# Performance work log

Measured on AMD Instinct MI355X. Metric: run time of the kernel, lower is better.

## Reference

```python
import jax, jax.numpy as jnp
import numpy as np

B, G, K = 16, 5000, 256
NUM_CELLS, HID = 100, 64
STEPS, ALPHA = 10, 0.1


def setup_inputs() -> dict:
    key = jax.random.key(0)
    ks = jax.random.split(key, 10)
    ctl = jax.random.normal(ks[0], (B, G), dtype=jnp.float32)
    drug_targets = jax.random.uniform(ks[1], (B, G), dtype=jnp.float32)
    cell_idx = jax.random.randint(ks[2], (B,), 0, NUM_CELLS)
    drug_fp = jax.random.normal(ks[3], (B, 128), dtype=jnp.float32)
    # gene->module membership matrix (constructor constant M_gk)
    M = jax.random.uniform(ks[4], (G, K), dtype=jnp.float32)
    # module-module adjacency (constructor constant A_kk), column-normalized for stability
    A = jax.random.uniform(ks[5], (K, K), dtype=jnp.float32)
    A = A / jnp.sum(A, axis=0, keepdims=True)
    # shared Dense(hidden_dim, relu): input feature dim is 3 (ctl, t, z_gene stacked)
    W1 = jax.random.normal(ks[6], (3, HID), dtype=jnp.float32) * 0.5
    b1 = jnp.zeros((HID,), dtype=jnp.float32)
    cell_emb = jax.random.normal(ks[7], (NUM_CELLS, HID), dtype=jnp.float32) * 0.05
    W2 = jax.random.normal(ks[8], (HID, 1), dtype=jnp.float32) * 0.1
    b2 = jnp.zeros((1,), dtype=jnp.float32)
    return {"ctl": ctl, "drug_targets": drug_targets, "cell_idx": cell_idx,
            "drug_fp": drug_fp, "M": M, "A": A, "W1": W1, "b1": b1,
            "cell_emb": cell_emb, "W2": W2, "b2": b2}


def reference(ctl, drug_targets, cell_idx, drug_fp, M, A, W1, b1, cell_emb, W2, b2):
    t = drug_targets                                   # [B, G]
    # max-pool gene targets into modules: max_g t[b,g] * M[g,k]
    t_mod = jnp.max(t[:, :, None] * M[None, :, :], axis=1)   # [B, K]
    # APPNP propagation: Z = (1-alpha) * Z @ A + alpha * S, fixed 10 steps
    Z = t_mod
    for _ in range(STEPS):
        Z = (1.0 - ALPHA) * (Z @ A) + ALPHA * t_mod
    z_gene = Z @ M.T                                   # [B, G]
    x = jnp.stack([ctl, t, z_gene], axis=-1)           # [B, G, 3]
    h = jax.nn.relu(x @ W1 + b1)                       # [B, G, HID]
    h = h + cell_emb[cell_idx][:, None, :]             # broadcast cell embedding
    y = jnp.squeeze(h @ W2 + b2, axis=-1)              # [B, G]
    return y
```

## Files before the change

kernel.cpp:

```cpp
#include <hip/hip_runtime.h>

#define G 5000
#define K 256
#define BATCH 16
#define HID 64
#define STEPS 10
#define NC 125
#define GPER 40

__global__ void maxpool_kernel(const float* __restrict__ t,
                               const float* __restrict__ M,
                               const float* __restrict__ A,
                               float* __restrict__ partials,
                               float* __restrict__ awarm) {
    __shared__ float tl[GPER][8];
    const int c  = blockIdx.x >> 1;
    const int bg = blockIdx.x & 1;
    const int b0 = bg * 8;
    const int k  = threadIdx.x;
    const int g0 = c * GPER;

    float4 aw = make_float4(0.f, 0.f, 0.f, 0.f);
    if (k < 64)
        aw = ((const float4*)A)[((size_t)blockIdx.x * 64 + k) & 16383];

    for (int i = k; i < GPER * 8; i += 256) {
        int gi = i >> 3, b = i & 7;
        tl[gi][b] = t[(b0 + b) * G + g0 + gi];
    }
    __syncthreads();

    float mx[8];
#pragma unroll
    for (int b = 0; b < 8; ++b) mx[b] = 0.f;

#pragma unroll 4
    for (int gi = 0; gi < GPER; ++gi) {
        float mg = M[(size_t)(g0 + gi) * K + k];
#pragma unroll
        for (int b = 0; b < 8; ++b)
            mx[b] = fmaxf(mx[b], tl[gi][b] * mg);
    }
#pragma unroll
    for (int b = 0; b < 8; ++b)
        partials[((size_t)c * BATCH + b0 + b) * K + k] = mx[b];

    if (k < 64) awarm[k] = aw.x + aw.y + aw.z + aw.w;
}

__global__ __launch_bounds__(1024, 4)
void appnp_fused(const float* __restrict__ partials,
                 const float* __restrict__ A,
                 const int* __restrict__ cell_idx,
                 const float* __restrict__ cell_emb,
                 const float* __restrict__ W2,
                 const float* __restrict__ b2,
                 float* __restrict__ Zfin,
                 float* __restrict__ ce_dot) {
    __shared__ float4 zb[2][K / 4];
    __shared__ float  Sm[K];
    __shared__ float  red[4][K];
    __shared__ float  ce_red[HID];

    const int b  = blockIdx.x;
    const int t  = threadIdx.x;
    const int k  = t & 255;
    const int jc = t >> 8;
    const int j0 = jc * 64;

    float Areg[64];
#pragma unroll
    for (int jj = 0; jj < 64; ++jj)
        Areg[jj] = A[(size_t)(j0 + jj) * K + k];

    {
        int c0 = jc * 32, c1 = min(NC, c0 + 32);
        float m = 0.f;
        for (int c = c0; c < c1; ++c)
            m = fmaxf(m, partials[((size_t)c * BATCH + b) * K + k]);
        red[jc][k] = m;
    }
    if (t < HID) {
        int ci = cell_idx[b];
        ce_red[t] = cell_emb[ci * HID + t] * W2[t];
    }
    __syncthreads();
    if (jc == 0) {
        float s = fmaxf(fmaxf(red[0][k], red[1][k]), fmaxf(red[2][k], red[3][k]));
        Sm[k] = s;
        ((float*)zb)[k] = s;
    }
    if (t == 0) {
        float s = b2[0];
        for (int h = 0; h < HID; ++h) s += ce_red[h];
        ce_dot[b] = s;
    }
    __syncthreads();

    for (int s = 0; s < STEPS; ++s) {
        const float4* cur4 = zb[s & 1] + (j0 >> 2);
        float*        nxt  = (float*)zb[(s + 1) & 1];
        float acc = 0.f;
#pragma unroll
        for (int q = 0; q < 16; ++q) {
            float4 c4 = cur4[q];
            acc = fmaf(c4.x, Areg[4 * q + 0], acc);
            acc = fmaf(c4.y, Areg[4 * q + 1], acc);
            acc = fmaf(c4.z, Areg[4 * q + 2], acc);
            acc = fmaf(c4.w, Areg[4 * q + 3], acc);
        }
        red[jc][k] = acc;
        __syncthreads();
        if (jc == 0)
            nxt[k] = 0.9f * (red[0][k] + red[1][k] + red[2][k] + red[3][k])
                   + 0.1f * Sm[k];
        __syncthreads();
    }
    if (jc == 0) Zfin[b * K + k] = ((float*)zb)[k];
}

__global__ void final_kernel(const float* __restrict__ ctl,
                             const float* __restrict__ t_in,
                             const float* __restrict__ Z,
                             const float* __restrict__ M,
                             const float* __restrict__ W1,
                             const float* __restrict__ b1,
                             const float* __restrict__ W2,
                             const float* __restrict__ ce_dot,
                             float* __restrict__ out) {
    __shared__ float4 zl[BATCH * (K / 4)];
    __shared__ float4 wpack[HID];
    __shared__ float  w2l[HID];
    __shared__ float  cel[BATCH];

    const int t = threadIdx.x;
    const float4* Z4 = (const float4*)Z;
    for (int i = t; i < BATCH * (K / 4); i += 256) zl[i] = Z4[i];
    if (t < HID) {
        wpack[t] = make_float4(W1[t], W1[HID + t], W1[2 * HID + t], b1[t]);
        w2l[t] = W2[t];
    }
    if (t < BATCH) cel[t] = ce_dot[t];
    __syncthreads();

    const int gl = t & 63;
    const int bg = t >> 6;
    const int g = blockIdx.x * 64 + gl;
    if (g >= G) return;

    float acc[4] = {0.f, 0.f, 0.f, 0.f};
    const float4* M4 = (const float4*)(M + (size_t)g * K);
#pragma unroll 4
    for (int k4 = 0; k4 < K / 4; ++k4) {
        float4 m4 = M4[k4];
#pragma unroll
        for (int i = 0; i < 4; ++i) {
            float4 z4 = zl[(bg * 4 + i) * (K / 4) + k4];
            acc[i] = fmaf(m4.x, z4.x, acc[i]);
            acc[i] = fmaf(m4.y, z4.y, acc[i]);
            acc[i] = fmaf(m4.z, z4.z, acc[i]);
            acc[i] = fmaf(m4.w, z4.w, acc[i]);
        }
    }

    float cv[4], tv[4], y[4];
#pragma unroll
    for (int i = 0; i < 4; ++i) {
        int b = bg * 4 + i;
        cv[i] = ctl[b * G + g];
        tv[i] = t_in[b * G + g];
        y[i] = cel[b];
    }
#pragma unroll 4
    for (int h = 0; h < HID; ++h) {
        float4 w = wpack[h];
        float w2h = w2l[h];
#pragma unroll
        for (int i = 0; i < 4; ++i) {
            float pre = w.w;
            pre = fmaf(cv[i], w.x, pre);
            pre = fmaf(tv[i], w.y, pre);
            pre = fmaf(acc[i], w.z, pre);
            pre = fmaxf(pre, 0.f);
            y[i] = fmaf(pre, w2h, y[i]);
        }
    }
#pragma unroll
    for (int i = 0; i < 4; ++i)
        out[(bg * 4 + i) * G + g] = y[i];
}

extern "C" void kernel_launch(void* const* d_in, const int* in_sizes, int n_in,
                              void* d_out, int out_size, void* d_ws, size_t ws_size,
                              hipStream_t stream) {
    const float* ctl      = (const float*)d_in[0];
    const float* tgt      = (const float*)d_in[1];
    const int*   cell_idx = (const int*)d_in[2];
    const float* M        = (const float*)d_in[4];
    const float* A        = (const float*)d_in[5];
    const float* W1       = (const float*)d_in[6];
    const float* b1       = (const float*)d_in[7];
    const float* cell_emb = (const float*)d_in[8];
    const float* W2       = (const float*)d_in[9];
    const float* b2       = (const float*)d_in[10];
    float* out = (float*)d_out;

    float* partials = (float*)d_ws;
    float* Zfin  = partials + (size_t)NC * BATCH * K;
    float* ce    = Zfin + BATCH * K;
    float* awarm = ce + BATCH;

    maxpool_kernel<<<NC * 2, 256, 0, stream>>>(tgt, M, A, partials, awarm);
    appnp_fused<<<BATCH, 1024, 0, stream>>>(partials, A, cell_idx, cell_emb,
                                            W2, b2, Zfin, ce);
    final_kernel<<<(G + 63) / 64, 256, 0, stream>>>(ctl, tgt, Zfin, M, W1, b1,
                                                    W2, ce, out);
}
```

Baseline: 115.1 us.

## Cover all batches per maxpool block and read Z via scalar loads

The maxpool kernel now launches one block per 20-gene chunk covering all 16 batches, where before it used two blocks per 40-gene chunk with 8 batches each. Each M element is loaded once for all batches, halving M reads, but there are twice as many partial chunks for the APPNP kernel to reduce. The final kernel drops the shared-memory staging of Z and reads Z straight from global memory using a wave-uniform batch group (readfirstlane), so those loads can become scalar/broadcast loads. This removes a shared-memory fill and a barrier dependency, at the risk of more global or scalar-cache traffic in the inner loop.

New measurement: 121.1 us. 1.05x slower.

```diff
diff --git a/kernel.cpp b/kernel.cpp
--- a/kernel.cpp
+++ b/kernel.cpp
@@ -5,18 +5,16 @@
 #define BATCH 16
 #define HID 64
 #define STEPS 10
-#define NC 125
-#define GPER 40
+#define NC 250
+#define GPER 20
 
 __global__ void maxpool_kernel(const float* __restrict__ t,
                                const float* __restrict__ M,
                                const float* __restrict__ A,
                                float* __restrict__ partials,
                                float* __restrict__ awarm) {
-    __shared__ float tl[GPER][8];
-    const int c  = blockIdx.x >> 1;
-    const int bg = blockIdx.x & 1;
-    const int b0 = bg * 8;
+    __shared__ float tl[GPER][BATCH];
+    const int c  = blockIdx.x;
     const int k  = threadIdx.x;
     const int g0 = c * GPER;
 
@@ -24,26 +22,26 @@
     if (k < 64)
         aw = ((const float4*)A)[((size_t)blockIdx.x * 64 + k) & 16383];
 
-    for (int i = k; i < GPER * 8; i += 256) {
-        int gi = i >> 3, b = i & 7;
-        tl[gi][b] = t[(b0 + b) * G + g0 + gi];
-    }
-    __syncthreads();
-
-    float mx[8];
-#pragma unroll
-    for (int b = 0; b < 8; ++b) mx[b] = 0.f;
+    for (int i = k; i < GPER * BATCH; i += 256) {
+        int gi = i >> 4, b = i & 15;
+        tl[gi][b] = t[b * G + g0 + gi];
+    }
+    __syncthreads();
+
+    float mx[BATCH];
+#pragma unroll
+    for (int b = 0; b < BATCH; ++b) mx[b] = 0.f;
 
 #pragma unroll 4
     for (int gi = 0; gi < GPER; ++gi) {
         float mg = M[(size_t)(g0 + gi) * K + k];
 #pragma unroll
-        for (int b = 0; b < 8; ++b)
+        for (int b = 0; b < BATCH; ++b)
             mx[b] = fmaxf(mx[b], tl[gi][b] * mg);
     }
 #pragma unroll
-    for (int b = 0; b < 8; ++b)
-        partials[((size_t)c * BATCH + b0 + b) * K + k] = mx[b];
+    for (int b = 0; b < BATCH; ++b)
+        partials[((size_t)c * BATCH + b) * K + k] = mx[b];
 
     if (k < 64) awarm[k] = aw.x + aw.y + aw.z + aw.w;
 }
@@ -74,7 +72,8 @@
         Areg[jj] = A[(size_t)(j0 + jj) * K + k];
 
     {
-        int c0 = jc * 32, c1 = min(NC, c0 + 32);
+        const int CPJ = (NC + 3) / 4;
+        int c0 = jc * CPJ, c1 = min(NC, c0 + CPJ);
         float m = 0.f;
         for (int c = c0; c < c1; ++c)
             m = fmaxf(m, partials[((size_t)c * BATCH + b) * K + k]);
@@ -128,14 +127,11 @@
                              const float* __restrict__ W2,
                              const float* __restrict__ ce_dot,
                              float* __restrict__ out) {
-    __shared__ float4 zl[BATCH * (K / 4)];
     __shared__ float4 wpack[HID];
     __shared__ float  w2l[HID];
     __shared__ float  cel[BATCH];
 
     const int t = threadIdx.x;
-    const float4* Z4 = (const float4*)Z;
-    for (int i = t; i < BATCH * (K / 4); i += 256) zl[i] = Z4[i];
     if (t < HID) {
         wpack[t] = make_float4(W1[t], W1[HID + t], W1[2 * HID + t], b1[t]);
         w2l[t] = W2[t];
@@ -144,9 +140,11 @@
     __syncthreads();
 
     const int gl = t & 63;
-    const int bg = t >> 6;
-    const int g = blockIdx.x * 64 + gl;
+    const int bg = __builtin_amdgcn_readfirstlane(t >> 6);
+    const int g  = blockIdx.x * 64 + gl;
     if (g >= G) return;
+
+    const float4* Zw = (const float4*)(Z + (size_t)bg * 4 * K);
 
     float acc[4] = {0.f, 0.f, 0.f, 0.f};
     const float4* M4 = (const float4*)(M + (size_t)g * K);
@@ -155,7 +153,7 @@
         float4 m4 = M4[k4];
 #pragma unroll
         for (int i = 0; i < 4; ++i) {
-            float4 z4 = zl[(bg * 4 + i) * (K / 4) + k4];
+            float4 z4 = Zw[i * (K / 4) + k4];
             acc[i] = fmaf(m4.x, z4.x, acc[i]);
             acc[i] = fmaf(m4.y, z4.y, acc[i]);
             acc[i] = fmaf(m4.z, z4.z, acc[i]);
@@ -210,7 +208,7 @@
     float* ce    = Zfin + BATCH * K;
     float* awarm = ce + BATCH;
 
-    maxpool_kernel<<<NC * 2, 256, 0, stream>>>(tgt, M, A, partials, awarm);
+    maxpool_kernel<<<NC, 256, 0, stream>>>(tgt, M, A, partials, awarm);
     appnp_fused<<<BATCH, 1024, 0, stream>>>(partials, A, cell_idx, cell_emb,
                                             W2, b2, Zfin, ce);
     final_kernel<<<(G + 63) / 64, 256, 0, stream>>>(ctl, tgt, Zfin, M, W1, b1,
```
